# Kernel optimization log

Measured on AMD Instinct MI355X. Metric: run time of the kernel, lower is better.

The kernel has to match this reference:

```python
import jax, jax.numpy as jnp
import numpy as np
import math

NUM_EMBED = 1024
EMBED_FEATS = 256
IN_FEATS = 512
COMMITMENT_COST = 0.25
B, T = 16, 4096


def setup_inputs() -> dict:
    key = jax.random.key(0)
    k1, k2, k3, k4 = jax.random.split(key, 4)
    inputs = jax.random.normal(k1, (B, IN_FEATS, T), dtype=jnp.float32)
    # Conv1d(kernel_size=1) == per-position linear: weight [E, C_in], bias [E]
    proj_w = jax.random.normal(k2, (EMBED_FEATS, IN_FEATS), dtype=jnp.float32) / np.sqrt(IN_FEATS)
    proj_b = jax.random.normal(k3, (EMBED_FEATS,), dtype=jnp.float32) * 0.01
    embed = jax.random.normal(k4, (NUM_EMBED, EMBED_FEATS), dtype=jnp.float32)
    return {"inputs": inputs, "proj_w": proj_w, "proj_b": proj_b, "embed": embed}


def reference(inputs, proj_w, proj_b, embed):
    sg = jax.lax.stop_gradient
    b, c_in, t = inputs.shape
    # 1x1 conv projection then transpose(1,-1): [B, T, E]
    x = jnp.einsum('bct,ec->bte', inputs, proj_w) + proj_b
    flat = x.reshape(-1, EMBED_FEATS)  # [B*T, E]
    d2 = (jnp.sum(flat * flat, axis=1, keepdims=True)
          + jnp.sum(embed * embed, axis=1)
          - 2.0 * flat @ embed.T)  # [B*T, num_embed]
    q_idx = jnp.argmin(d2, axis=1)  # [B*T]
    # one-hot @ embed == direct gather (same math, same gradient structure)
    z_q = embed[q_idx].reshape(x.shape)  # [B, T, E]
    vq_loss = jnp.mean((z_q - sg(x)) ** 2)
    commitment_loss = jnp.mean((sg(z_q) - x) ** 2)
    loss = vq_loss + COMMITMENT_COST * commitment_loss
    z_q_st = x + sg(z_q - x)  # straight-through
    n_tokens = flat.shape[0]
    probs = jnp.zeros((NUM_EMBED,), dtype=jnp.float32).at[q_idx].add(1.0) / n_tokens
    log_perplexity = -jnp.sum(probs * jnp.log(probs + 1e-10))
    num_spatial = n_tokens / b
    kldiv_r = math.log(NUM_EMBED) * num_spatial * jnp.ones((b, 1), dtype=jnp.float32)
    z_q_out = jnp.swapaxes(z_q_st, 1, 2)  # [B, E, T]
    return z_q_out, loss, kldiv_r, log_perplexity
```

## Files before the change

kernel.cpp:

```cpp
#include <hip/hip_runtime.h>
#include <hip/hip_bf16.h>
#include <math.h>

#define TT   4096
#define BB   16
#define NTOK 65536
#define CIN  512
#define EF   256
#define NE   1024

typedef __attribute__((ext_vector_type(8))) short bf16x8;
typedef __attribute__((ext_vector_type(4))) float f32x4;

static __device__ __forceinline__ unsigned short f2bf(float f) {
  unsigned int u = __float_as_uint(f);
  u += 0x7fffu + ((u >> 16) & 1u);
  return (unsigned short)(u >> 16);
}

#define GLL(gsrc, ldst) \
  __builtin_amdgcn_global_load_lds((const __attribute__((address_space(1))) void*)(gsrc), \
                                   (__attribute__((address_space(3))) void*)(ldst), 16, 0, 0)

__global__ __launch_bounds__(256) void k_prep(const float* __restrict__ Wf,
                                              const float* __restrict__ Ef,
                                              unsigned short* __restrict__ Wbf,
                                              unsigned short* __restrict__ Ebf,
                                              float* __restrict__ e_norm) {
  int bid = blockIdx.x;
  if (bid < 512) {
    int i = bid * 256 + threadIdx.x;
    Wbf[i] = f2bf(Wf[i]);
  } else if (bid < 1536) {
    int i = (bid - 512) * 256 + threadIdx.x;
    Ebf[i] = f2bf(-2.0f * Ef[i]);
  } else {
    int w = threadIdx.x >> 6, l = threadIdx.x & 63;
    int k = (bid - 1536) * 4 + w;
    const float4 v4 = ((const float4*)(Ef + (size_t)k * EF))[l];
    float s = v4.x * v4.x + v4.y * v4.y + v4.z * v4.z + v4.w * v4.w;
    for (int off = 32; off; off >>= 1) s += __shfl_down(s, off);
    if (l == 0) e_norm[k] = s;
  }
}

__global__ __launch_bounds__(512, 2) void k_fused(const float* __restrict__ in,
                                                  const unsigned short* __restrict__ Wbf,
                                                  const float* __restrict__ bias,
                                                  const unsigned short* __restrict__ Ebf,
                                                  const float* __restrict__ e_norm,
                                                  int* __restrict__ bi_out,
                                                  unsigned int* __restrict__ hist,
                                                  float* __restrict__ sse) {
  __shared__ unsigned short lds[32768];
  unsigned short* as_ = lds;
  unsigned short* bs  = lds + 8192;
  unsigned short* xs  = lds;

  int tid = threadIdx.x;
  int w = tid >> 6, l = tid & 63;
  int l15 = l & 15, quad = l >> 4;
  int tq = w & 1, eq = w >> 1;
  int cg = w & 3, th = w >> 2;
  int tok0 = blockIdx.x * 128;
  const float* src = in + (size_t)(tok0 >> 12) * CIN * TT + (tok0 & 4095);

  f32x4 acc[4][4];
#pragma unroll
  for (int a = 0; a < 4; ++a)
#pragma unroll
    for (int b = 0; b < 4; ++b) acc[a][b] = (f32x4){0.f, 0.f, 0.f, 0.f};

  float v[16];
  {
    const float* s0 = src + (size_t)(cg * 16) * TT + th * 64 + l;
#pragma unroll
    for (int i = 0; i < 16; ++i) v[i] = s0[(size_t)i * TT];
  }
  for (int ks = 0; ks < 8; ++ks) {
    int k0 = ks * 64;
#pragma unroll
    for (int i = 0; i < 4; ++i) {
      int g = i * 512 + tid;
      int row = g >> 3, pc = g & 7, lc = pc ^ (row & 7);
      GLL(Wbf + (size_t)row * CIN + k0 + lc * 8, bs + g * 8);
    }
    int trow = th * 64 + l;
#pragma unroll
    for (int cc = 0; cc < 2; ++cc) {
      alignas(16) unsigned short tmp[8];
#pragma unroll
      for (int j = 0; j < 8; ++j) tmp[j] = f2bf(v[cc * 8 + j]);
      int c8 = cg * 2 + cc;
      int pc = c8 ^ (trow & 7);
      *(bf16x8*)(as_ + trow * 64 + pc * 8) = *(const bf16x8*)tmp;
    }
    __syncthreads();
    if (ks < 7) {
      const float* s0 = src + (size_t)(k0 + 64 + cg * 16) * TT + th * 64 + l;
#pragma unroll
      for (int i = 0; i < 16; ++i) v[i] = s0[(size_t)i * TT];
    }
#pragma unroll
    for (int kstep = 0; kstep < 2; ++kstep) {
      int ck = kstep * 4 + quad;
      bf16x8 af[4], bfr[4];
#pragma unroll
      for (int msub = 0; msub < 4; ++msub) {
        int row = tq * 64 + msub * 16 + l15;
        int pa = ck ^ (row & 7);
        af[msub] = *(const bf16x8*)(as_ + row * 64 + pa * 8);
      }
#pragma unroll
      for (int nsub = 0; nsub < 4; ++nsub) {
        int row = eq * 64 + nsub * 16 + l15;
        int pb = ck ^ (row & 7);
        bfr[nsub] = *(const bf16x8*)(bs + row * 64 + pb * 8);
      }
#pragma unroll
      for (int msub = 0; msub < 4; ++msub)
#pragma unroll
        for (int nsub = 0; nsub < 4; ++nsub)
          acc[msub][nsub] = __builtin_amdgcn_mfma_f32_16x16x32_bf16(af[msub], bfr[nsub],
                                                                    acc[msub][nsub], 0, 0, 0);
    }
    __syncthreads();
  }

  float xsq = 0.f;
#pragma unroll
  for (int nsub = 0; nsub < 4; ++nsub) {
    int e = eq * 64 + nsub * 16 + l15;
    float bv = bias[e];
    int cx = e >> 3;
#pragma unroll
    for (int msub = 0; msub < 4; ++msub)
#pragma unroll
      for (int reg = 0; reg < 4; ++reg) {
        int m = tq * 64 + msub * 16 + quad * 4 + reg;
        float x = acc[msub][nsub][reg] + bv;
        xsq += x * x;
        int pcx = cx ^ (m & 31);
        xs[m * 256 + pcx * 8 + (e & 7)] = f2bf(x);
      }
  }
  __syncthreads();

  int g3 = w & 3, h = w >> 2;
  bf16x8 af[2][8];
#pragma unroll
  for (int msub = 0; msub < 2; ++msub)
#pragma unroll
    for (int kst = 0; kst < 8; ++kst) {
      int row = g3 * 32 + msub * 16 + l15;
      int c32 = kst * 4 + quad;
      int pcx = c32 ^ (row & 31);
      af[msub][kst] = *(const bf16x8*)(xs + row * 256 + pcx * 8);
    }
  __syncthreads();

#pragma unroll
  for (int i = 0; i < 4; ++i) {
    int g = i * 512 + tid;
    int row = g >> 5, pcc = g & 31, lc = pcc ^ (row & 31);
    GLL(Ebf + (size_t)row * EF + lc * 8, lds + g * 8);
  }
  float enn[2];
  enn[0] = e_norm[h * 32 + l15];
  enn[1] = e_norm[h * 32 + 16 + l15];
  __syncthreads();

  float best_v[2][4];
  int best_i[2][4];
#pragma unroll
  for (int a = 0; a < 2; ++a)
#pragma unroll
    for (int b = 0; b < 4; ++b) { best_v[a][b] = 3.0e38f; best_i[a][b] = 0; }

  for (int chunk = 0; chunk < 16; ++chunk) {
    int p = chunk & 1;
    int c0 = chunk * 64;
    unsigned short* eb = lds + p * 16384;
    if (chunk < 15) {
      unsigned short* ebn = lds + (p ^ 1) * 16384;
#pragma unroll
      for (int i = 0; i < 4; ++i) {
        int g = i * 512 + tid;
        int row = g >> 5, pcc = g & 31, lc = pcc ^ (row & 31);
        GLL(Ebf + (size_t)(c0 + 64 + row) * EF + lc * 8, ebn + g * 8);
      }
    }
    f32x4 dacc[2][2];
#pragma unroll
    for (int nsub = 0; nsub < 2; ++nsub) {
      float en = enn[nsub];
#pragma unroll
      for (int msub = 0; msub < 2; ++msub) dacc[msub][nsub] = (f32x4){en, en, en, en};
    }
    if (chunk < 15) {
      enn[0] = e_norm[c0 + 64 + h * 32 + l15];
      enn[1] = e_norm[c0 + 64 + h * 32 + 16 + l15];
    }
#pragma unroll
    for (int nsub = 0; nsub < 2; ++nsub) {
      int r = h * 32 + nsub * 16 + l15;
#pragma unroll
      for (int kst = 0; kst < 8; ++kst) {
        int cc = kst * 4 + quad;
        int pc = cc ^ (r & 31);
        bf16x8 bfr = *(const bf16x8*)(eb + r * 256 + pc * 8);
        dacc[0][nsub] = __builtin_amdgcn_mfma_f32_16x16x32_bf16(af[0][kst], bfr,
                                                                dacc[0][nsub], 0, 0, 0);
        dacc[1][nsub] = __builtin_amdgcn_mfma_f32_16x16x32_bf16(af[1][kst], bfr,
                                                                dacc[1][nsub], 0, 0, 0);
      }
    }
#pragma unroll
    for (int msub = 0; msub < 2; ++msub)
#pragma unroll
      for (int nsub = 0; nsub < 2; ++nsub) {
        int code = c0 + h * 32 + nsub * 16 + l15;
#pragma unroll
        for (int reg = 0; reg < 4; ++reg) {
          float vv = dacc[msub][nsub][reg];
          if (vv < best_v[msub][reg]) { best_v[msub][reg] = vv; best_i[msub][reg] = code; }
        }
      }
    __syncthreads();
  }

#pragma unroll
  for (int msub = 0; msub < 2; ++msub)
#pragma unroll
    for (int reg = 0; reg < 4; ++reg) {
      float vv = best_v[msub][reg];
      int idx = best_i[msub][reg];
#pragma unroll
      for (int off = 8; off; off >>= 1) {
        float ov = __shfl_xor(vv, off, 16);
        int oi = __shfl_xor(idx, off, 16);
        if (ov < vv || (ov == vv && oi < idx)) { vv = ov; idx = oi; }
      }
      best_v[msub][reg] = vv;
      best_i[msub][reg] = idx;
    }
  float* red_v = (float*)lds;
  int* red_i = (int*)lds + 256;
  float* xred = (float*)lds + 512;
  float* svred = (float*)lds + 520;
  if (l15 == 0) {
#pragma unroll
    for (int msub = 0; msub < 2; ++msub)
#pragma unroll
      for (int reg = 0; reg < 4; ++reg) {
        int tokloc = g3 * 32 + msub * 16 + quad * 4 + reg;
        red_v[h * 128 + tokloc] = best_v[msub][reg];
        red_i[h * 128 + tokloc] = best_i[msub][reg];
      }
  }
  for (int off = 32; off; off >>= 1) xsq += __shfl_down(xsq, off);
  if (l == 0) xred[w] = xsq;
  __syncthreads();
  if (tid < 128) {
    float v0 = red_v[tid], v1 = red_v[128 + tid];
    int i0 = red_i[tid], i1 = red_i[128 + tid];
    float vv; int idx;
    if (v1 < v0 || (v1 == v0 && i1 < i0)) { vv = v1; idx = i1; } else { vv = v0; idx = i0; }
    bi_out[tok0 + tid] = idx;
    atomicAdd(&hist[idx], 1u);
    for (int off = 32; off; off >>= 1) vv += __shfl_down(vv, off);
    if ((tid & 63) == 0) svred[tid >> 6] = vv;
  }
  __syncthreads();
  if (tid == 0) {
    float tot = svred[0] + svred[1];
#pragma unroll
    for (int i = 0; i < 8; ++i) tot += xred[i];
    atomicAdd(sse, tot);
  }
}

__global__ __launch_bounds__(256) void k_gather(const float* __restrict__ embed,
                                                const int* __restrict__ bi,
                                                float* __restrict__ out) {
  __shared__ float zq[128 * 65];
  __shared__ int idxs[128];
  int tid = threadIdx.x;
  int tok0 = blockIdx.x * 128;
  int e0 = blockIdx.y * 64;
  if (tid < 128) idxs[tid] = bi[tok0 + tid];
  __syncthreads();
  int l15 = tid & 15, tg = tid >> 4;
  for (int r = 0; r < 8; ++r) {
    int tl = r * 16 + tg;
    const float4 v = *(const float4*)(embed + (size_t)idxs[tl] * EF + e0 + l15 * 4);
    float* zr = zq + tl * 65 + l15 * 4;
    zr[0] = v.x; zr[1] = v.y; zr[2] = v.z; zr[3] = v.w;
  }
  __syncthreads();
  int b = tok0 >> 12, t0 = tok0 & 4095;
  int tl4 = (tid & 31) * 4;
  for (int r = 0; r < 8; ++r) {
    int e = r * 8 + (tid >> 5);
    float4 v;
    v.x = zq[(tl4 + 0) * 65 + e];
    v.y = zq[(tl4 + 1) * 65 + e];
    v.z = zq[(tl4 + 2) * 65 + e];
    v.w = zq[(tl4 + 3) * 65 + e];
    *(float4*)(out + ((size_t)(b * EF + e0 + e) << 12) + t0 + tl4) = v;
  }
}

__global__ __launch_bounds__(256) void k_final(const unsigned int* __restrict__ hist,
                                               const float* __restrict__ sse,
                                               float* __restrict__ out) {
  __shared__ float red[4];
  int tid = threadIdx.x;
  float local = 0.f;
  for (int i = tid; i < NE; i += 256) {
    float p = (float)hist[i] * (1.0f / 65536.0f);
    local -= p * logf(p + 1e-10f);
  }
  for (int off = 32; off; off >>= 1) local += __shfl_down(local, off);
  if ((tid & 63) == 0) red[tid >> 6] = local;
  __syncthreads();
  if (tid == 0) {
    float lp = red[0] + red[1] + red[2] + red[3];
    out[16777216] = 1.25f * sse[0] / 16777216.0f;
    out[16777233] = lp;
  }
  if (tid < 16) out[16777217 + tid] = 6.93147180559945f * 4096.0f;
}

extern "C" void kernel_launch(void* const* d_in, const int* in_sizes, int n_in,
                              void* d_out, int out_size, void* d_ws, size_t ws_size,
                              hipStream_t stream) {
  const float* inputs = (const float*)d_in[0];
  const float* proj_w = (const float*)d_in[1];
  const float* proj_b = (const float*)d_in[2];
  const float* embed = (const float*)d_in[3];
  float* out = (float*)d_out;
  char* ws = (char*)d_ws;

  unsigned short* Wbf  = (unsigned short*)(ws);
  unsigned short* Ebf  = (unsigned short*)(ws + 262144);
  float* e_norm        = (float*)(ws + 786432);
  int* bi              = (int*)(ws + 790528);
  unsigned int* hist   = (unsigned int*)(ws + 1052672);
  float* sse           = (float*)(ws + 1056768);
  if (ws_size < 1056772) return;

  hipMemsetAsync(ws + 1052672, 0, 4100, stream);

  k_prep<<<1792, 256, 0, stream>>>(proj_w, embed, Wbf, Ebf, e_norm);
  k_fused<<<512, 512, 0, stream>>>(inputs, Wbf, proj_b, Ebf, e_norm, bi, hist, sse);
  k_gather<<<dim3(512, 4), 256, 0, stream>>>(embed, bi, out);
  k_final<<<1, 256, 0, stream>>>(hist, sse, out);
}
```

Baseline: 295.7 us.

## Split projection GEMM from distance search and fuse gather into distance kernel

Splits the fused projection+distance kernel into two. The projection GEMM now runs on 64-token tiles with 256 threads and writes bf16 x to a global workspace. A new distance kernel reads x from that workspace, does the argmin over the codebook with each wave covering all 64 codes per chunk, and then gathers and writes the transposed z_q output itself, removing the separate gather kernel and the index buffer. This trades an extra 32 MB round trip of bf16 activations for smaller, more parallel GEMM blocks, no cross-wave argmin merge, and one less launch.

```diff
diff --git a/kernel.cpp b/kernel.cpp
--- a/kernel.cpp
+++ b/kernel.cpp
@@ -44,25 +44,20 @@
   }
 }
 
-__global__ __launch_bounds__(512, 2) void k_fused(const float* __restrict__ in,
+__global__ __launch_bounds__(256, 2) void k_gemm1(const float* __restrict__ in,
                                                   const unsigned short* __restrict__ Wbf,
                                                   const float* __restrict__ bias,
-                                                  const unsigned short* __restrict__ Ebf,
-                                                  const float* __restrict__ e_norm,
-                                                  int* __restrict__ bi_out,
-                                                  unsigned int* __restrict__ hist,
+                                                  unsigned short* __restrict__ x_bf,
                                                   float* __restrict__ sse) {
-  __shared__ unsigned short lds[32768];
+  __shared__ unsigned short lds[20480];
   unsigned short* as_ = lds;
-  unsigned short* bs  = lds + 8192;
+  unsigned short* bs  = lds + 4096;
   unsigned short* xs  = lds;
 
   int tid = threadIdx.x;
   int w = tid >> 6, l = tid & 63;
   int l15 = l & 15, quad = l >> 4;
-  int tq = w & 1, eq = w >> 1;
-  int cg = w & 3, th = w >> 2;
-  int tok0 = blockIdx.x * 128;
+  int tok0 = blockIdx.x * 64;
   const float* src = in + (size_t)(tok0 >> 12) * CIN * TT + (tok0 & 4095);
 
   f32x4 acc[4][4];
@@ -73,31 +68,30 @@
 
   float v[16];
   {
-    const float* s0 = src + (size_t)(cg * 16) * TT + th * 64 + l;
+    const float* s0 = src + (size_t)(w * 16) * TT + l;
 #pragma unroll
     for (int i = 0; i < 16; ++i) v[i] = s0[(size_t)i * TT];
   }
   for (int ks = 0; ks < 8; ++ks) {
     int k0 = ks * 64;
 #pragma unroll
-    for (int i = 0; i < 4; ++i) {
-      int g = i * 512 + tid;
+    for (int i = 0; i < 8; ++i) {
+      int g = i * 256 + tid;
       int row = g >> 3, pc = g & 7, lc = pc ^ (row & 7);
       GLL(Wbf + (size_t)row * CIN + k0 + lc * 8, bs + g * 8);
     }
-    int trow = th * 64 + l;
 #pragma unroll
     for (int cc = 0; cc < 2; ++cc) {
       alignas(16) unsigned short tmp[8];
 #pragma unroll
       for (int j = 0; j < 8; ++j) tmp[j] = f2bf(v[cc * 8 + j]);
-      int c8 = cg * 2 + cc;
-      int pc = c8 ^ (trow & 7);
-      *(bf16x8*)(as_ + trow * 64 + pc * 8) = *(const bf16x8*)tmp;
+      int c8 = w * 2 + cc;
+      int pc = c8 ^ (l & 7);
+      *(bf16x8*)(as_ + l * 64 + pc * 8) = *(const bf16x8*)tmp;
     }
     __syncthreads();
     if (ks < 7) {
-      const float* s0 = src + (size_t)(k0 + 64 + cg * 16) * TT + th * 64 + l;
+      const float* s0 = src + (size_t)(k0 + 64 + w * 16) * TT + l;
 #pragma unroll
       for (int i = 0; i < 16; ++i) v[i] = s0[(size_t)i * TT];
     }
@@ -107,13 +101,13 @@
       bf16x8 af[4], bfr[4];
 #pragma unroll
       for (int msub = 0; msub < 4; ++msub) {
-        int row = tq * 64 + msub * 16 + l15;
+        int row = msub * 16 + l15;
         int pa = ck ^ (row & 7);
         af[msub] = *(const bf16x8*)(as_ + row * 64 + pa * 8);
       }
 #pragma unroll
       for (int nsub = 0; nsub < 4; ++nsub) {
-        int row = eq * 64 + nsub * 16 + l15;
+        int row = w * 64 + nsub * 16 + l15;
         int pb = ck ^ (row & 7);
         bfr[nsub] = *(const bf16x8*)(bs + row * 64 + pb * 8);
       }
@@ -130,14 +124,14 @@
   float xsq = 0.f;
 #pragma unroll
   for (int nsub = 0; nsub < 4; ++nsub) {
-    int e = eq * 64 + nsub * 16 + l15;
+    int e = w * 64 + nsub * 16 + l15;
     float bv = bias[e];
     int cx = e >> 3;
 #pragma unroll
     for (int msub = 0; msub < 4; ++msub)
 #pragma unroll
       for (int reg = 0; reg < 4; ++reg) {
-        int m = tq * 64 + msub * 16 + quad * 4 + reg;
+        int m = msub * 16 + quad * 4 + reg;
         float x = acc[msub][nsub][reg] + bv;
         xsq += x * x;
         int pcx = cx ^ (m & 31);
@@ -145,29 +139,56 @@
       }
   }
   __syncthreads();
-
-  int g3 = w & 3, h = w >> 2;
+#pragma unroll
+  for (int i = 0; i < 8; ++i) {
+    int g = i * 256 + tid;
+    int m = g >> 5, c = g & 31;
+    int pcx = c ^ (m & 31);
+    bf16x8 val = *(const bf16x8*)(xs + m * 256 + pcx * 8);
+    *(bf16x8*)(x_bf + (size_t)(tok0 + m) * EF + c * 8) = val;
+  }
+  __shared__ float xred[4];
+  for (int off = 32; off; off >>= 1) xsq += __shfl_down(xsq, off);
+  if (l == 0) xred[w] = xsq;
+  __syncthreads();
+  if (tid == 0) atomicAdd(sse, xred[0] + xred[1] + xred[2] + xred[3]);
+}
+
+__global__ __launch_bounds__(256, 1) void k_dist(const unsigned short* __restrict__ x_bf,
+                                                 const unsigned short* __restrict__ Ebf,
+                                                 const float* __restrict__ e_norm,
+                                                 const float* __restrict__ embed,
+                                                 float* __restrict__ out,
+                                                 unsigned int* __restrict__ hist,
+                                                 float* __restrict__ sse) {
+  __shared__ unsigned short lds[32768];
+  float* zq    = (float*)lds;
+  int* idxs    = (int*)(lds + 30720);
+  float* svred = (float*)(lds + 31488);
+
+  int tid = threadIdx.x;
+  int w = tid >> 6, l = tid & 63;
+  int l15 = l & 15, quad = l >> 4;
+  int tok0 = blockIdx.x * 128;
+
   bf16x8 af[2][8];
 #pragma unroll
   for (int msub = 0; msub < 2; ++msub)
 #pragma unroll
     for (int kst = 0; kst < 8; ++kst) {
-      int row = g3 * 32 + msub * 16 + l15;
-      int c32 = kst * 4 + quad;
-      int pcx = c32 ^ (row & 31);
-      af[msub][kst] = *(const bf16x8*)(xs + row * 256 + pcx * 8);
-    }
-  __syncthreads();
-
-#pragma unroll
-  for (int i = 0; i < 4; ++i) {
-    int g = i * 512 + tid;
+      int row = tok0 + w * 32 + msub * 16 + l15;
+      af[msub][kst] = *(const bf16x8*)(x_bf + (size_t)row * EF + (kst * 4 + quad) * 8);
+    }
+
+#pragma unroll
+  for (int i = 0; i < 8; ++i) {
+    int g = i * 256 + tid;
     int row = g >> 5, pcc = g & 31, lc = pcc ^ (row & 31);
     GLL(Ebf + (size_t)row * EF + lc * 8, lds + g * 8);
   }
-  float enn[2];
-  enn[0] = e_norm[h * 32 + l15];
-  enn[1] = e_norm[h * 32 + 16 + l15];
+  float enn[4];
+#pragma unroll
+  for (int nsub = 0; nsub < 4; ++nsub) enn[nsub] = e_norm[nsub * 16 + l15];
   __syncthreads();
 
   float best_v[2][4];
@@ -178,37 +199,35 @@
     for (int b = 0; b < 4; ++b) { best_v[a][b] = 3.0e38f; best_i[a][b] = 0; }
 
   for (int chunk = 0; chunk < 16; ++chunk) {
-    int p = chunk & 1;
     int c0 = chunk * 64;
-    unsigned short* eb = lds + p * 16384;
+    unsigned short* eb = lds + (chunk & 1) * 16384;
     if (chunk < 15) {
-      unsigned short* ebn = lds + (p ^ 1) * 16384;
-#pragma unroll
-      for (int i = 0; i < 4; ++i) {
-        int g = i * 512 + tid;
+      unsigned short* ebn = lds + ((chunk & 1) ^ 1) * 16384;
+#pragma unroll
+      for (int i = 0; i < 8; ++i) {
+        int g = i * 256 + tid;
         int row = g >> 5, pcc = g & 31, lc = pcc ^ (row & 31);
         GLL(Ebf + (size_t)(c0 + 64 + row) * EF + lc * 8, ebn + g * 8);
       }
     }
-    f32x4 dacc[2][2];
-#pragma unroll
-    for (int nsub = 0; nsub < 2; ++nsub) {
+    f32x4 dacc[2][4];
+#pragma unroll
+    for (int nsub = 0; nsub < 4; ++nsub) {
       float en = enn[nsub];
-#pragma unroll
-      for (int msub = 0; msub < 2; ++msub) dacc[msub][nsub] = (f32x4){en, en, en, en};
+      dacc[0][nsub] = (f32x4){en, en, en, en};
+      dacc[1][nsub] = (f32x4){en, en, en, en};
     }
     if (chunk < 15) {
-      enn[0] = e_norm[c0 + 64 + h * 32 + l15];
-      enn[1] = e_norm[c0 + 64 + h * 32 + 16 + l15];
-    }
-#pragma unroll
-    for (int nsub = 0; nsub < 2; ++nsub) {
-      int r = h * 32 + nsub * 16 + l15;
+#pragma unroll
+      for (int nsub = 0; nsub < 4; ++nsub) enn[nsub] = e_norm[c0 + 64 + nsub * 16 + l15];
+    }
+#pragma unroll
+    for (int nsub = 0; nsub < 4; ++nsub) {
+      int n = nsub * 16 + l15;
 #pragma unroll
       for (int kst = 0; kst < 8; ++kst) {
-        int cc = kst * 4 + quad;
-        int pc = cc ^ (r & 31);
-        bf16x8 bfr = *(const bf16x8*)(eb + r * 256 + pc * 8);
+        int pc = (kst * 4 + quad) ^ (n & 31);
+        bf16x8 bfr = *(const bf16x8*)(eb + n * 256 + pc * 8);
         dacc[0][nsub] = __builtin_amdgcn_mfma_f32_16x16x32_bf16(af[0][kst], bfr,
                                                                 dacc[0][nsub], 0, 0, 0);
         dacc[1][nsub] = __builtin_amdgcn_mfma_f32_16x16x32_bf16(af[1][kst], bfr,
@@ -218,8 +237,8 @@
 #pragma unroll
     for (int msub = 0; msub < 2; ++msub)
 #pragma unroll
-      for (int nsub = 0; nsub < 2; ++nsub) {
-        int code = c0 + h * 32 + nsub * 16 + l15;
+      for (int nsub = 0; nsub < 4; ++nsub) {
+        int code = c0 + nsub * 16 + l15;
 #pragma unroll
         for (int reg = 0; reg < 4; ++reg) {
           float vv = dacc[msub][nsub][reg];
@@ -229,6 +248,7 @@
     __syncthreads();
   }
 
+  float sv = 0.f;
 #pragma unroll
   for (int msub = 0; msub < 2; ++msub)
 #pragma unroll
@@ -241,73 +261,40 @@
         int oi = __shfl_xor(idx, off, 16);
         if (ov < vv || (ov == vv && oi < idx)) { vv = ov; idx = oi; }
       }
-      best_v[msub][reg] = vv;
-      best_i[msub][reg] = idx;
-    }
-  float* red_v = (float*)lds;
-  int* red_i = (int*)lds + 256;
-  float* xred = (float*)lds + 512;
-  float* svred = (float*)lds + 520;
-  if (l15 == 0) {
-#pragma unroll
-    for (int msub = 0; msub < 2; ++msub)
-#pragma unroll
-      for (int reg = 0; reg < 4; ++reg) {
-        int tokloc = g3 * 32 + msub * 16 + quad * 4 + reg;
-        red_v[h * 128 + tokloc] = best_v[msub][reg];
-        red_i[h * 128 + tokloc] = best_i[msub][reg];
-      }
-  }
-  for (int off = 32; off; off >>= 1) xsq += __shfl_down(xsq, off);
-  if (l == 0) xred[w] = xsq;
-  __syncthreads();
-  if (tid < 128) {
-    float v0 = red_v[tid], v1 = red_v[128 + tid];
-    int i0 = red_i[tid], i1 = red_i[128 + tid];
-    float vv; int idx;
-    if (v1 < v0 || (v1 == v0 && i1 < i0)) { vv = v1; idx = i1; } else { vv = v0; idx = i0; }
-    bi_out[tok0 + tid] = idx;
-    atomicAdd(&hist[idx], 1u);
-    for (int off = 32; off; off >>= 1) vv += __shfl_down(vv, off);
-    if ((tid & 63) == 0) svred[tid >> 6] = vv;
-  }
-  __syncthreads();
-  if (tid == 0) {
-    float tot = svred[0] + svred[1];
-#pragma unroll
-    for (int i = 0; i < 8; ++i) tot += xred[i];
-    atomicAdd(sse, tot);
-  }
-}
-
-__global__ __launch_bounds__(256) void k_gather(const float* __restrict__ embed,
-                                                const int* __restrict__ bi,
-                                                float* __restrict__ out) {
-  __shared__ float zq[128 * 65];
-  __shared__ int idxs[128];
-  int tid = threadIdx.x;
-  int tok0 = blockIdx.x * 128;
-  int e0 = blockIdx.y * 64;
-  if (tid < 128) idxs[tid] = bi[tok0 + tid];
-  __syncthreads();
-  int l15 = tid & 15, tg = tid >> 4;
-  for (int r = 0; r < 8; ++r) {
-    int tl = r * 16 + tg;
-    const float4 v = *(const float4*)(embed + (size_t)idxs[tl] * EF + e0 + l15 * 4);
-    float* zr = zq + tl * 65 + l15 * 4;
-    zr[0] = v.x; zr[1] = v.y; zr[2] = v.z; zr[3] = v.w;
-  }
-  __syncthreads();
+      if (l15 == 0) {
+        int m = w * 32 + msub * 16 + quad * 4 + reg;
+        idxs[m] = idx;
+        atomicAdd(&hist[idx], 1u);
+        sv += vv;
+      }
+    }
+  for (int off = 32; off; off >>= 1) sv += __shfl_down(sv, off);
+  if (l == 0) svred[w] = sv;
+  __syncthreads();
+  if (tid == 0) atomicAdd(sse, svred[0] + svred[1] + svred[2] + svred[3]);
+
   int b = tok0 >> 12, t0 = tok0 & 4095;
-  int tl4 = (tid & 31) * 4;
-  for (int r = 0; r < 8; ++r) {
-    int e = r * 8 + (tid >> 5);
-    float4 v;
-    v.x = zq[(tl4 + 0) * 65 + e];
-    v.y = zq[(tl4 + 1) * 65 + e];
-    v.z = zq[(tl4 + 2) * 65 + e];
-    v.w = zq[(tl4 + 3) * 65 + e];
-    *(float4*)(out + ((size_t)(b * EF + e0 + e) << 12) + t0 + tl4) = v;
+  int tg = tid >> 4;
+  for (int pass = 0; pass < 4; ++pass) {
+    int e0 = pass * 64;
+    __syncthreads();
+    for (int r = 0; r < 8; ++r) {
+      int tl = r * 16 + tg;
+      const float4 vv = *(const float4*)(embed + (size_t)idxs[tl] * EF + e0 + l15 * 4);
+      float* zr = zq + tl * 65 + l15 * 4;
+      zr[0] = vv.x; zr[1] = vv.y; zr[2] = vv.z; zr[3] = vv.w;
+    }
+    __syncthreads();
+    int tl4 = (tid & 31) * 4;
+    for (int r = 0; r < 8; ++r) {
+      int e = r * 8 + (tid >> 5);
+      float4 vv;
+      vv.x = zq[(tl4 + 0) * 65 + e];
+      vv.y = zq[(tl4 + 1) * 65 + e];
+      vv.z = zq[(tl4 + 2) * 65 + e];
+      vv.w = zq[(tl4 + 3) * 65 + e];
+      *(float4*)(out + ((size_t)(b * EF + e0 + e) << 12) + t0 + tl4) = vv;
+    }
   }
 }
 
@@ -342,18 +329,18 @@
   float* out = (float*)d_out;
   char* ws = (char*)d_ws;
 
-  unsigned short* Wbf  = (unsigned short*)(ws);
-  unsigned short* Ebf  = (unsigned short*)(ws + 262144);
-  float* e_norm        = (float*)(ws + 786432);
-  int* bi              = (int*)(ws + 790528);
-  unsigned int* hist   = (unsigned int*)(ws + 1052672);
-  float* sse           = (float*)(ws + 1056768);
-  if (ws_size < 1056772) return;
-
-  hipMemsetAsync(ws + 1052672, 0, 4100, stream);
+  unsigned short* x_bf = (unsigned short*)(ws);
+  unsigned short* Wbf  = (unsigned short*)(ws + 33554432);
+  unsigned short* Ebf  = (unsigned short*)(ws + 33816576);
+  float* e_norm        = (float*)(ws + 34340864);
+  unsigned int* hist   = (unsigned int*)(ws + 34344960);
+  float* sse           = (float*)(ws + 34349056);
+  if (ws_size < 34349060) return;
+
+  hipMemsetAsync(ws + 34344960, 0, 4100, stream);
 
   k_prep<<<1792, 256, 0, stream>>>(proj_w, embed, Wbf, Ebf, e_norm);
-  k_fused<<<512, 512, 0, stream>>>(inputs, Wbf, proj_b, Ebf, e_norm, bi, hist, sse);
-  k_gather<<<dim3(512, 4), 256, 0, stream>>>(embed, bi, out);
+  k_gemm1<<<1024, 256, 0, stream>>>(inputs, Wbf, proj_b, x_bf, sse);
+  k_dist<<<512, 256, 0, stream>>>(x_bf, Ebf, e_norm, embed, out, hist, sse);
   k_final<<<1, 256, 0, stream>>>(hist, sse, out);
 }
```

Measured after the change: 306.9 us. 1.04x slower.
